# Kernel tuning notes

Measured on AMD Instinct MI355X. Metric: run time of the kernel, lower is better.

Reference implementation:

```python
import jax, jax.numpy as jnp
import numpy as np

SQRT_2PI = (2.0 * 3.14159) ** 0.5  # matches torch.jit.script gaussian constant


def setup_inputs() -> dict:
    key = jax.random.key(0)
    ks = jax.random.split(key, 7)
    B, N, R, K, H, HEADS = 4, 256, 4, 128, 512, 32
    rpe = jax.random.uniform(ks[0], (B, N, N, R), dtype=jnp.float32) * 5.0
    means = jax.random.uniform(ks[1], (R, K), dtype=jnp.float32, minval=0.0, maxval=3.0)
    stds = jax.random.uniform(ks[2], (R, K), dtype=jnp.float32, minval=0.0, maxval=3.0)
    W1 = jax.random.normal(ks[3], (H, R * K), dtype=jnp.float32) * (1.0 / (R * K) ** 0.5)
    b1 = jax.random.normal(ks[4], (H,), dtype=jnp.float32) * 0.01
    W2 = jax.random.normal(ks[5], (HEADS, H), dtype=jnp.float32) * (1.0 / H ** 0.5)
    b2 = jax.random.normal(ks[6], (HEADS,), dtype=jnp.float32) * 0.01
    return {"rpe": rpe, "means": means, "stds": stds, "W1": W1, "b1": b1, "W2": W2, "b2": b2}


def reference(rpe, means, stds, W1, b1, W2, b2):
    # GaussianLayer: (B,N,N,R) -> (B,N,N,R*K)
    std = jnp.abs(stds) + 0.01                      # (R,K)
    x = rpe[..., None]                              # (B,N,N,R,1)
    g = jnp.exp(-0.5 * ((x - means) / std) ** 2) / (SQRT_2PI * std)  # (B,N,N,R,K)
    B, N = rpe.shape[0], rpe.shape[1]
    g = g.reshape(B, N, N, -1)                      # (B,N,N,R*K)
    # NonLinear MLP: Linear -> gelu(exact) -> Linear
    h = jax.nn.gelu(jnp.einsum('bmnf,hf->bmnh', g, W1) + b1, approximate=False)
    out = jnp.einsum('bmnh,oh->bmno', h, W2) + b2   # (B,N,N,heads)
    # permute BATCH_HEAD_NODE_NODE = (0,3,1,2)
    return jnp.transpose(out, (0, 3, 1, 2))
```

## Files before the change

### kernel.cpp

```cpp
#include <hip/hip_runtime.h>
#include <hip/hip_bf16.h>

typedef __attribute__((ext_vector_type(8))) short bfrag8;
typedef __attribute__((ext_vector_type(4))) float f32x4;
typedef __attribute__((ext_vector_type(4))) unsigned int u32x4;

#define IS2_SCALE 0.84932180028801907f
#define W1_SCALE  0.46971724f

#if __has_builtin(__builtin_amdgcn_exp2f)
#define GEXP(x) __builtin_amdgcn_exp2f(x)
#else
__device__ __forceinline__ float gexp_asm(float x) {
  float r; asm("v_exp_f32 %0, %1" : "=v"(r) : "v"(x)); return r;
}
#define GEXP(x) gexp_asm(x)
#endif

__device__ __forceinline__ unsigned short f2bf(float x) {
  union { float f; unsigned u; } v; v.f = x;
  unsigned r = v.u + 0x7fffu + ((v.u >> 16) & 1u);
  return (unsigned short)(r >> 16);
}
__device__ __forceinline__ unsigned cvtpk(float lo, float hi) {
  unsigned r;
  asm("v_cvt_pk_bf16_f32 %0, %1, %2" : "=v"(r) : "v"(lo), "v"(hi));
  return r;
}
__device__ __forceinline__ float rcpa(float x) {
  float r; asm("v_rcp_f32 %0, %1" : "=v"(r) : "v"(x)); return r;
}
__device__ __forceinline__ float gelu_fast(float x) {
  float x2 = x * x;
  float w = __builtin_fmaf(x2, -0.1029488f, -2.3022078f);
  float e = GEXP(x * w);
  return x * rcpa(e + 1.0f);
}

__device__ __forceinline__ void gauss_frags(const f32x4* prm4, const f32x4 xa, const f32x4 xb,
                                            int kb, int lg, bfrag8* A0, bfrag8* A1) {
  const int k0 = kb * 32 + lg * 8;
  const float x0 = xa[kb >> 2], x1 = xb[kb >> 2];
  unsigned pk0[4], pk1[4];
#pragma unroll
  for (int q = 0; q < 4; ++q) {
    f32x4 P = prm4[(k0 >> 1) + q];
    float u00 = __builtin_fmaf(x0, P[1], P[0]);
    float u01 = __builtin_fmaf(x0, P[3], P[2]);
    float u10 = __builtin_fmaf(x1, P[1], P[0]);
    float u11 = __builtin_fmaf(x1, P[3], P[2]);
    pk0[q] = cvtpk(P[1] * GEXP(-(u00 * u00)), P[3] * GEXP(-(u01 * u01)));
    pk1[q] = cvtpk(P[1] * GEXP(-(u10 * u10)), P[3] * GEXP(-(u11 * u11)));
  }
  u32x4 av0 = {pk0[0], pk0[1], pk0[2], pk0[3]};
  u32x4 av1 = {pk1[0], pk1[1], pk1[2], pk1[3]};
  *A0 = __builtin_bit_cast(bfrag8, av0);
  *A1 = __builtin_bit_cast(bfrag8, av1);
}

__global__ void prep_kernel(const float* __restrict__ means, const float* __restrict__ stds,
                            const float* __restrict__ W1, const float* __restrict__ W2,
                            unsigned short* __restrict__ W1bf, unsigned short* __restrict__ W2bf,
                            float* __restrict__ prm ) {
  int t = blockIdx.x * blockDim.x + threadIdx.x;
  int stride = gridDim.x * blockDim.x;
  for (int i = t; i < 512 * 512; i += stride) W1bf[i] = f2bf(W1[i] * W1_SCALE);
  for (int i = t; i < 32 * 512; i += stride) W2bf[i] = f2bf(W2[i]);
  for (int i = t; i < 512; i += stride) {
    float s = fabsf(stds[i]) + 0.01f;
    float is2 = (1.0f / s) * IS2_SCALE;
    prm[2 * i] = -means[i] * is2;
    prm[2 * i + 1] = is2;
  }
}

__global__ __launch_bounds__(1024, 4) void fused_kernel(
    const float* __restrict__ rpe, const unsigned short* __restrict__ W1bf,
    const unsigned short* __restrict__ W2bf, const float* __restrict__ prm,
    const float* __restrict__ b1, const float* __restrict__ b2,
    float* __restrict__ out) {
  __shared__ __attribute__((aligned(16))) char lds[131072 + 4096 + 2048 + 2048];
  float* prm_s = (float*)(lds + 131072);
  float* rpe_s = (float*)(lds + 131072 + 4096);
  float* b1_s  = (float*)(lds + 131072 + 4096 + 2048);

  const int tid = threadIdx.x;
  const int rb = blockIdx.x * 128;

  if (tid < 512) rpe_s[tid] = rpe[rb * 4 + tid];
  prm_s[tid] = prm[tid];
  if (tid < 512) b1_s[tid] = b1[tid];

  int goff[2];
#pragma unroll
  for (int i = 0; i < 2; ++i) {
    int c = i * 1024 + tid;
    int j = ((c >> 6) << 4) + (c & 15);
    goff[i] = j * 512 + ((c >> 4) & 3) * 8;
  }
  const char* Wc = (const char*)W1bf;

#define STAGE(buf, kb)                                                          \
  {                                                                             \
    _Pragma("unroll") for (int i_ = 0; i_ < 2; ++i_) {                          \
      const void* gp = (const void*)(Wc + (size_t)goff[i_] * 2 + (kb) * 64);    \
      void* lp = (void*)(lds + (buf) * 32768 + i_ * 16384 + tid * 16);          \
      __builtin_amdgcn_global_load_lds(                                         \
          (const __attribute__((address_space(1))) void*)gp,                    \
          (__attribute__((address_space(3))) void*)lp, 16, 0, 0);               \
    }                                                                           \
  }

  STAGE(0, 0);
  STAGE(1, 1);
  __syncthreads();

  const int w = tid >> 6, l = tid & 63;
  const int lr = l & 15, lg = l >> 4;
  const int mw = w >> 2, nw = w & 3;
  const int r0 = mw * 32 + lr;

  const f32x4 xa = *(const f32x4*)&rpe_s[r0 * 4];
  const f32x4 xb = *(const f32x4*)&rpe_s[(r0 + 16) * 4];
  const f32x4* prm4 = (const f32x4*)prm_s;

  f32x4 zv = {0.f, 0.f, 0.f, 0.f};
  f32x4 acc[2][8];
#pragma unroll
  for (int mf = 0; mf < 2; ++mf)
#pragma unroll
    for (int nf = 0; nf < 8; ++nf) acc[mf][nf] = zv;

  bfrag8 fA[4], fB[4];
  {
    const char* Bb = lds + nw * 8192 + lg * 256 + lr * 16;
#pragma unroll
    for (int nf = 0; nf < 4; ++nf) fA[nf] = *(const bfrag8*)(Bb + nf * 1024);
  }
  bfrag8 a0, a1;
  gauss_frags(prm4, xa, xb, 0, lg, &a0, &a1);

#pragma unroll
  for (int kb = 0; kb < 16; ++kb) {
    asm volatile("s_waitcnt vmcnt(0)" ::: "memory");
    __builtin_amdgcn_s_barrier();
    __builtin_amdgcn_sched_barrier(0);
    if (kb < 14) STAGE((kb + 2) % 3, kb + 2);

    const char* Bb = lds + (kb % 3) * 32768 + nw * 8192 + lg * 256 + lr * 16;
    __builtin_amdgcn_s_setprio(1);
#pragma unroll
    for (int nf = 0; nf < 4; ++nf) fB[nf] = *(const bfrag8*)(Bb + (nf + 4) * 1024);
#pragma unroll
    for (int nf = 0; nf < 4; ++nf) {
      acc[0][nf] = __builtin_amdgcn_mfma_f32_16x16x32_bf16(a0, fA[nf], acc[0][nf], 0, 0, 0);
      acc[1][nf] = __builtin_amdgcn_mfma_f32_16x16x32_bf16(a1, fA[nf], acc[1][nf], 0, 0, 0);
    }
    __builtin_amdgcn_s_setprio(0);
    __builtin_amdgcn_sched_barrier(0);

    __builtin_amdgcn_s_setprio(1);
    if (kb < 15) {
      const char* Bn = lds + ((kb + 1) % 3) * 32768 + nw * 8192 + lg * 256 + lr * 16;
#pragma unroll
      for (int nf = 0; nf < 4; ++nf) fA[nf] = *(const bfrag8*)(Bn + nf * 1024);
    }
#pragma unroll
    for (int nf = 0; nf < 4; ++nf) {
      acc[0][nf + 4] = __builtin_amdgcn_mfma_f32_16x16x32_bf16(a0, fB[nf], acc[0][nf + 4], 0, 0, 0);
      acc[1][nf + 4] = __builtin_amdgcn_mfma_f32_16x16x32_bf16(a1, fB[nf], acc[1][nf + 4], 0, 0, 0);
    }
    __builtin_amdgcn_s_setprio(0);
    if (kb < 15) gauss_frags(prm4, xa, xb, kb + 1, lg, &a0, &a1);
    __builtin_amdgcn_sched_barrier(0);
  }
  __syncthreads();

  unsigned short* hbuf = (unsigned short*)lds;
#pragma unroll
  for (int mf = 0; mf < 2; ++mf) {
#pragma unroll
    for (int nf = 0; nf < 8; nf += 2) {
      int col0 = nw * 128 + nf * 16 + lr;
      int col1 = col0 + 16;
      float bb0 = b1_s[col0], bb1 = b1_s[col1];
#pragma unroll
      for (int bi = 0; bi < 4; ++bi) {
        float g0 = gelu_fast(acc[mf][nf][bi] + bb0);
        float g1 = gelu_fast(acc[mf][nf + 1][bi] + bb1);
        unsigned pr = cvtpk(g0, g1);
        int hrow = mw * 32 + mf * 16 + lg * 4 + bi;
        int base = hrow * 1024, sw = (hrow & 7) << 4;
        *(unsigned short*)((char*)hbuf + base + ((col0 * 2) ^ sw)) = (unsigned short)pr;
        *(unsigned short*)((char*)hbuf + base + ((col1 * 2) ^ sw)) = (unsigned short)(pr >> 16);
      }
    }
  }
  __syncthreads();

  const int rt = w >> 1, ct = w & 1;
  f32x4 acc2 = zv;
  const int row2 = rt * 16 + lr;
  for (int kb = 0; kb < 16; ++kb) {
    int cb = (kb * 64 + lg * 16) ^ ((row2 & 7) << 4);
    bfrag8 a = *(const bfrag8*)((char*)hbuf + row2 * 1024 + cb);
    bfrag8 b = *(const bfrag8*)(W2bf + (size_t)(ct * 16 + lr) * 512 + kb * 32 + lg * 8);
    acc2 = __builtin_amdgcn_mfma_f32_16x16x32_bf16(a, b, acc2, 0, 0, 0);
  }
  float b2v = b2[ct * 16 + lr];
  __syncthreads();

  float* ob = (float*)lds;
#pragma unroll
  for (int bi = 0; bi < 4; ++bi)
    ob[(rt * 16 + lg * 4 + bi) * 33 + (ct * 16 + lr)] = acc2[bi] + b2v;
  __syncthreads();

  const int bI = rb >> 16, mI = (rb >> 8) & 255, n0 = rb & 255;
  float* obase = out + ((size_t)(bI * 32) * 256 + mI) * 256 + n0;
#pragma unroll
  for (int p = 0; p < 4; ++p) {
    int e = tid + p * 1024;
    int o = e >> 7, i = e & 127;
    obase[(size_t)o * 65536 + i] = ob[i * 33 + o];
  }
#undef STAGE
}

extern "C" void kernel_launch(void* const* d_in, const int* in_sizes, int n_in,
                              void* d_out, int out_size, void* d_ws, size_t ws_size,
                              hipStream_t stream) {
  const float* rpe   = (const float*)d_in[0];
  const float* means = (const float*)d_in[1];
  const float* stds  = (const float*)d_in[2];
  const float* W1    = (const float*)d_in[3];
  const float* b1    = (const float*)d_in[4];
  const float* W2    = (const float*)d_in[5];
  const float* b2    = (const float*)d_in[6];
  float* out = (float*)d_out;

  char* ws = (char*)d_ws;
  unsigned short* W1bf = (unsigned short*)ws;
  unsigned short* W2bf = (unsigned short*)(ws + 524288);
  float* prm = (float*)(ws + 557056);

  prep_kernel<<<256, 256, 0, stream>>>(means, stds, W1, W2, W1bf, W2bf, prm);
  fused_kernel<<<2048, 1024, 0, stream>>>(rpe, W1bf, W2bf, prm, b1, b2, out);
}
```

Measured before the change: 271.8 us.

## Compute Gaussian A-fragments once per row group and share via LDS ring

Before this change, all four waves that share a row group (same mw) computed the same Gaussian-feature bf16 A fragments with exp, so the transcendental work was done four times over. Now only the wave with mw==nw computes them, two k-blocks ahead, into a three-slot LDS ring in the unused space above the W1 staging buffers. The other waves read the fragments from LDS, relying on the existing per-iteration barrier for visibility. This cuts redundant VALU/exp work per SIMD, since the producer waves land on different SIMDs. The cost is extra LDS traffic, an explicit lgkmcnt wait, and uneven per-wave work that the barrier may expose.

New measurement: 257.4 us (median of 3 runs). 1.06x faster.

```diff
diff --git a/kernel.cpp b/kernel.cpp
--- a/kernel.cpp
+++ b/kernel.cpp
@@ -80,6 +80,7 @@
     const float* __restrict__ b1, const float* __restrict__ b2,
     float* __restrict__ out) {
   __shared__ __attribute__((aligned(16))) char lds[131072 + 4096 + 2048 + 2048];
+  char*  gsl   = lds + 98304;
   float* prm_s = (float*)(lds + 131072);
   float* rpe_s = (float*)(lds + 131072 + 4096);
   float* b1_s  = (float*)(lds + 131072 + 4096 + 2048);
@@ -113,17 +114,30 @@
 
   STAGE(0, 0);
   STAGE(1, 1);
-  __syncthreads();
 
   const int w = tid >> 6, l = tid & 63;
   const int lr = l & 15, lg = l >> 4;
   const int mw = w >> 2, nw = w & 3;
   const int r0 = mw * 32 + lr;
+  const bool prod = (mw == nw);
 
   const f32x4 xa = *(const f32x4*)&rpe_s[r0 * 4];
   const f32x4 xb = *(const f32x4*)&rpe_s[(r0 + 16) * 4];
   const f32x4* prm4 = (const f32x4*)prm_s;
 
+  char* gbase = gsl + mw * 2048 + lg * 256 + lr * 16;
+
+  __syncthreads();
+
+  if (prod) {
+    bfrag8 t0, t1;
+    gauss_frags(prm4, xa, xb, 0, lg, &t0, &t1);
+    *(bfrag8*)(gbase) = t0;  *(bfrag8*)(gbase + 1024) = t1;
+    gauss_frags(prm4, xa, xb, 1, lg, &t0, &t1);
+    *(bfrag8*)(gbase + 8192) = t0;  *(bfrag8*)(gbase + 8192 + 1024) = t1;
+  }
+  __syncthreads();
+
   f32x4 zv = {0.f, 0.f, 0.f, 0.f};
   f32x4 acc[2][8];
 #pragma unroll
@@ -131,14 +145,14 @@
 #pragma unroll
     for (int nf = 0; nf < 8; ++nf) acc[mf][nf] = zv;
 
+  bfrag8 acur0 = *(const bfrag8*)(gbase);
+  bfrag8 acur1 = *(const bfrag8*)(gbase + 1024);
   bfrag8 fA[4], fB[4];
   {
     const char* Bb = lds + nw * 8192 + lg * 256 + lr * 16;
 #pragma unroll
     for (int nf = 0; nf < 4; ++nf) fA[nf] = *(const bfrag8*)(Bb + nf * 1024);
   }
-  bfrag8 a0, a1;
-  gauss_frags(prm4, xa, xb, 0, lg, &a0, &a1);
 
 #pragma unroll
   for (int kb = 0; kb < 16; ++kb) {
@@ -153,8 +167,8 @@
     for (int nf = 0; nf < 4; ++nf) fB[nf] = *(const bfrag8*)(Bb + (nf + 4) * 1024);
 #pragma unroll
     for (int nf = 0; nf < 4; ++nf) {
-      acc[0][nf] = __builtin_amdgcn_mfma_f32_16x16x32_bf16(a0, fA[nf], acc[0][nf], 0, 0, 0);
-      acc[1][nf] = __builtin_amdgcn_mfma_f32_16x16x32_bf16(a1, fA[nf], acc[1][nf], 0, 0, 0);
+      acc[0][nf] = __builtin_amdgcn_mfma_f32_16x16x32_bf16(acur0, fA[nf], acc[0][nf], 0, 0, 0);
+      acc[1][nf] = __builtin_amdgcn_mfma_f32_16x16x32_bf16(acur1, fA[nf], acc[1][nf], 0, 0, 0);
     }
     __builtin_amdgcn_s_setprio(0);
     __builtin_amdgcn_sched_barrier(0);
@@ -167,11 +181,23 @@
     }
 #pragma unroll
     for (int nf = 0; nf < 4; ++nf) {
-      acc[0][nf + 4] = __builtin_amdgcn_mfma_f32_16x16x32_bf16(a0, fB[nf], acc[0][nf + 4], 0, 0, 0);
-      acc[1][nf + 4] = __builtin_amdgcn_mfma_f32_16x16x32_bf16(a1, fB[nf], acc[1][nf + 4], 0, 0, 0);
+      acc[0][nf + 4] = __builtin_amdgcn_mfma_f32_16x16x32_bf16(acur0, fB[nf], acc[0][nf + 4], 0, 0, 0);
+      acc[1][nf + 4] = __builtin_amdgcn_mfma_f32_16x16x32_bf16(acur1, fB[nf], acc[1][nf + 4], 0, 0, 0);
     }
     __builtin_amdgcn_s_setprio(0);
-    if (kb < 15) gauss_frags(prm4, xa, xb, kb + 1, lg, &a0, &a1);
+
+    if (kb < 15) {
+      const char* gs = gbase + ((kb + 1) % 3) * 8192;
+      acur0 = *(const bfrag8*)(gs);
+      acur1 = *(const bfrag8*)(gs + 1024);
+    }
+    if (prod && kb < 14) {
+      bfrag8 t0, t1;
+      gauss_frags(prm4, xa, xb, kb + 2, lg, &t0, &t1);
+      char* gd = gbase + ((kb + 2) % 3) * 8192;
+      *(bfrag8*)(gd) = t0;  *(bfrag8*)(gd + 1024) = t1;
+      asm volatile("s_waitcnt lgkmcnt(0)" ::: "memory");
+    }
     __builtin_amdgcn_sched_barrier(0);
   }
   __syncthreads();
```
